# Performance work log

Hardware: AMD Instinct MI355X
Metric: run time of the kernel (lower is better)

## Reference

```python
import jax, jax.numpy as jnp
import numpy as np

DROP_PERCENT = 30  # a_percent passed in forward_construct_dynamic_ftr_map


def setup_inputs() -> dict:
    key = jax.random.key(0)
    # x: (b, w, n, h) = (batch, windows, nodes, feature/time)
    x = jax.random.normal(key, (8, 16, 400, 512), dtype=jnp.float32)
    return {"x": x}


def _dropedge(adj, percent):
    # adj: (B, n, n). Zero the `percent`% smallest-|value| entries per sample.
    # Matches torch's per-sample stable sort + scatter-zero, but batched.
    B, n, _ = adj.shape
    num_to_zero = int(n * n * percent / 100)
    if num_to_zero == 0:
        return adj
    flat = adj.reshape(B, n * n)
    # rank of each element in ascending |value| order (stable, like torch.sort)
    order = jnp.argsort(jnp.abs(flat), axis=-1)          # stable by default
    ranks = jnp.argsort(order, axis=-1)
    flat = jnp.where(ranks >= num_to_zero, flat, jnp.zeros((), flat.dtype))
    return flat.reshape(B, n, n)


def reference(x):
    b, w, n, h = x.shape
    xf = x.reshape(b * w, n, h)                 # rearrange 'b w n h -> (b w) n h'
    x_glb = xf.mean(axis=-1)                    # AdaptiveAvgPool1d(1)  -> (bw, n)
    x_max = xf.max(axis=-1)                     # AdaptiveMaxPool1d(1)  -> (bw, n)
    # bmm of (bw,n,1) @ (bw,1,n) == outer product per sample
    adj = jax.nn.sigmoid(x_glb[:, :, None] * x_max[:, None, :])  # (bw, n, n)
    dynamic_ftr_map = _dropedge(adj, DROP_PERCENT)
    return (xf, dynamic_ftr_map)
```

## Files before the change

### kernel.cpp

```cpp
#include <hip/hip_runtime.h>
#include <math.h>

#define HDIM  512
#define NSAMP 128
#define NN    400
#define NN2   160000
#define KZERO 48000
#define NROWS 51200
#define BPS   10
#define QPS   40000
#define QPB   4000
#define NBINS 12288
#define NWORDS 6144
#define BINBASE 0x3E000000u
#define BINSH 11
#define CANDCAP 1024

__device__ __forceinline__ float xla_expf(float x) {
  x = fminf(88.3762626647950f, fmaxf(-88.3762626647949f, x));
  float fx = floorf(fmaf(x, 1.44269504088896341f, 0.5f));
  x = fmaf(fx, -0.693359375f, x);
  x = fmaf(fx, 2.12194440e-4f, x);
  float z2 = __fmul_rn(x, x);
  float y = 1.9875691500e-4f;
  y = fmaf(y, x, 1.3981999507e-3f);
  y = fmaf(y, x, 8.3334519073e-3f);
  y = fmaf(y, x, 4.1665795894e-2f);
  y = fmaf(y, x, 1.6666665459e-1f);
  y = fmaf(y, x, 5.0000001201e-1f);
  y = fmaf(y, z2, x);
  y = __fadd_rn(y, 1.0f);
  int n = (int)fx;
  float p2n = __int_as_float((n + 127) << 23);
  return __fmul_rn(y, p2n);
}

__device__ __forceinline__ float sigf(float g, float m) {
  float z = __fmul_rn(g, m);
  float e = xla_expf(-z);
  float den = __fadd_rn(1.0f, e);
  return __fdiv_rn(1.0f, den);
}

__device__ __forceinline__ int binOf(unsigned int u) {
  if (u < BINBASE) return 0;
  unsigned int d = (u - BINBASE) >> BINSH;
  return d > (NBINS - 1) ? (NBINS - 1) : (int)d;
}

__global__ __launch_bounds__(256) void k_pool(const float* __restrict__ x,
                                              float* __restrict__ out0,
                                              float* __restrict__ glb,
                                              float* __restrict__ mx,
                                              unsigned int* __restrict__ zbase,
                                              int zwords) {
  int gid = blockIdx.x * 256 + threadIdx.x;
  if (gid < zwords) zbase[gid] = 0u;
  __shared__ float buf[4][512];
  const int wave = threadIdx.x >> 6;
  const int lane = threadIdx.x & 63;
  const int row  = blockIdx.x * 4 + wave;
  const float4* xr = reinterpret_cast<const float4*>(x) + (size_t)row * 128;
  float4* o = reinterpret_cast<float4*>(out0) + (size_t)row * 128;
  float4 a = xr[lane];
  float4 b = xr[lane + 64];
  o[lane]      = a;
  o[lane + 64] = b;
  reinterpret_cast<float4*>(buf[wave])[lane]      = a;
  reinterpret_cast<float4*>(buf[wave])[lane + 64] = b;
  float m = fmaxf(fmaxf(fmaxf(a.x, a.y), fmaxf(a.z, a.w)),
                  fmaxf(fmaxf(b.x, b.y), fmaxf(b.z, b.w)));
#pragma unroll
  for (int off = 32; off > 0; off >>= 1) m = fmaxf(m, __shfl_xor(m, off));
  __syncthreads();
  float r = 0.0f;
  if (lane < 8) {
    const float* p = buf[wave] + lane;
    r = p[0];
    for (int t = 1; t < 64; ++t) r = __fadd_rn(r, p[8 * t]);
    r = __fadd_rn(r, __shfl_xor(r, 4));
    r = __fadd_rn(r, __shfl_xor(r, 2));
    r = __fadd_rn(r, __shfl_xor(r, 1));
  }
  if (lane == 0) {
    glb[row] = __fmul_rn(r, 0.001953125f);
    mx[row]  = m;
  }
}

__global__ __launch_bounds__(256) void k_sig(const float* __restrict__ glb,
                                             const float* __restrict__ mx,
                                             unsigned int* __restrict__ adju,
                                             unsigned int* __restrict__ hist) {
  const int blk = blockIdx.x, b = blk / BPS, part = blk % BPS, t = threadIdx.x;
  __shared__ unsigned int lh[NWORDS];
  for (int k = t; k < NWORDS; k += 256) lh[k] = 0u;
  __syncthreads();
  const float* gb = glb + b * NN;
  const float4* mb = (const float4*)(mx + b * NN);
  uint4* base = (uint4*)adju + (size_t)b * QPS;
  const int qend = (part + 1) * QPB;
  for (int q = part * QPB + t; q < qend; q += 256) {
    int i  = q / 100;
    int jq = q - i * 100;
    float g = gb[i];
    float4 m4 = mb[jq];
    uint4 u;
    u.x = __float_as_uint(sigf(g, m4.x));
    u.y = __float_as_uint(sigf(g, m4.y));
    u.z = __float_as_uint(sigf(g, m4.z));
    u.w = __float_as_uint(sigf(g, m4.w));
    base[q] = u;
    int b0 = binOf(u.x), b1 = binOf(u.y), b2 = binOf(u.z), b3 = binOf(u.w);
    atomicAdd(&lh[b0 >> 1], 1u << ((b0 & 1) << 4));
    atomicAdd(&lh[b1 >> 1], 1u << ((b1 & 1) << 4));
    atomicAdd(&lh[b2 >> 1], 1u << ((b2 & 1) << 4));
    atomicAdd(&lh[b3 >> 1], 1u << ((b3 & 1) << 4));
  }
  __syncthreads();
  unsigned int* gh = hist + (size_t)b * NWORDS;
  for (int k = t; k < NWORDS; k += 256)
    if (lh[k]) atomicAdd(&gh[k], lh[k]);
}

__global__ __launch_bounds__(256) void k_scanBin(const unsigned int* __restrict__ hist,
                                                 unsigned int* __restrict__ stB,
                                                 unsigned int* __restrict__ stR) {
  const int b = blockIdx.x, t = threadIdx.x;
  const unsigned int* h = hist + (size_t)b * NWORDS;
  unsigned int w[24];
  unsigned int part = 0;
  for (int k = 0; k < 24; ++k) {
    w[k] = h[t * 24 + k];
    part += (w[k] & 0xffffu) + (w[k] >> 16);
  }
  const int lane = t & 63, wid = t >> 6;
  unsigned int inc = part;
  for (int off = 1; off < 64; off <<= 1) {
    unsigned int v = __shfl_up(inc, off);
    if (lane >= off) inc += v;
  }
  __shared__ unsigned int wsum[4], wbase[4];
  __shared__ int sB;
  __shared__ unsigned int sR;
  if (lane == 63) wsum[wid] = inc;
  __syncthreads();
  if (t == 0) {
    unsigned int c = 0;
    for (int i = 0; i < 4; ++i) { wbase[i] = c; c += wsum[i]; }
  }
  __syncthreads();
  unsigned int excl = wbase[wid] + inc - part;
  if (part > 0 && KZERO >= excl && KZERO < excl + part) {
    unsigned int c = excl;
    for (int k = 0; k < 24; ++k) {
      unsigned int lo = w[k] & 0xffffu, hi = w[k] >> 16;
      if ((unsigned)KZERO < c + lo) { sB = (t * 24 + k) * 2;     sR = KZERO - c; break; }
      c += lo;
      if ((unsigned)KZERO < c + hi) { sB = (t * 24 + k) * 2 + 1; sR = KZERO - c; break; }
      c += hi;
    }
  }
  __syncthreads();
  if (t == 0) { stB[b] = (unsigned int)sB; stR[b] = sR; }
}

__global__ __launch_bounds__(256) void k_cand(const unsigned int* __restrict__ adju,
                                              const unsigned int* __restrict__ stB,
                                              unsigned int* __restrict__ stNC,
                                              unsigned int* __restrict__ candI,
                                              unsigned int* __restrict__ candU) {
  const int blk = blockIdx.x, b = blk / BPS, part = blk % BPS, t = threadIdx.x;
  const int B = (int)stB[b];
  const uint4* base = (const uint4*)adju + (size_t)b * QPS;
  const int qend = (part + 1) * QPB;
  for (int q = part * QPB + t; q < qend; q += 256) {
    uint4 u = base[q];
    unsigned int uv[4] = {u.x, u.y, u.z, u.w};
#pragma unroll
    for (int k = 0; k < 4; ++k) {
      if (binOf(uv[k]) == B) {
        unsigned int pos = atomicAdd(&stNC[b], 1u);
        if (pos < CANDCAP) {
          candI[b * CANDCAP + pos] = (unsigned int)(q * 4 + k);
          candU[b * CANDCAP + pos] = uv[k];
        }
      }
    }
  }
}

__global__ __launch_bounds__(256) void k_final(unsigned int* __restrict__ adju,
                                               const unsigned int* __restrict__ stR,
                                               const unsigned int* __restrict__ stNC,
                                               const unsigned int* __restrict__ candI,
                                               const unsigned int* __restrict__ candU) {
  const int blk = blockIdx.x, b = blk / BPS, part = blk % BPS, t = threadIdx.x;
  __shared__ unsigned int cI[CANDCAP], cU[CANDCAP];
  __shared__ unsigned int sT, sIdx;
  int nc = (int)stNC[b];
  if (nc > CANDCAP) nc = CANDCAP;
  for (int i = t; i < nc; i += 256) {
    cI[i] = candI[b * CANDCAP + i];
    cU[i] = candU[b * CANDCAP + i];
  }
  if (t == 0) { sT = 0xFFFFFFFFu; sIdx = 0u; }
  __syncthreads();
  const unsigned int R = stR[b];
  for (int i = t; i < nc; i += 256) {
    unsigned int ui = cU[i], ii = cI[i];
    unsigned int rank = 0;
    for (int j = 0; j < nc; ++j)
      rank += (unsigned)((cU[j] < ui) || (cU[j] == ui && cI[j] < ii));
    if (rank == R) { sT = ui; sIdx = ii; }
  }
  __syncthreads();
  const unsigned int T = sT;
  const int idxT = (int)sIdx;
  uint4* base = (uint4*)adju + (size_t)b * QPS;
  const int qend = (part + 1) * QPB;
  for (int q = part * QPB + t; q < qend; q += 256) {
    uint4 u = base[q];
    int e0 = q * 4;
    uint4 v;
    v.x = (u.x < T || (u.x == T && (e0 + 0) < idxT)) ? 0u : u.x;
    v.y = (u.y < T || (u.y == T && (e0 + 1) < idxT)) ? 0u : u.y;
    v.z = (u.z < T || (u.z == T && (e0 + 2) < idxT)) ? 0u : u.z;
    v.w = (u.w < T || (u.w == T && (e0 + 3) < idxT)) ? 0u : u.w;
    if (v.x != u.x || v.y != u.y || v.z != u.z || v.w != u.w) base[q] = v;
  }
}

extern "C" void kernel_launch(void* const* d_in, const int* in_sizes, int n_in,
                              void* d_out, int out_size, void* d_ws, size_t ws_size,
                              hipStream_t stream) {
  const float* x = (const float*)d_in[0];
  float* out0 = (float*)d_out;
  unsigned int* adju = (unsigned int*)((float*)d_out + (size_t)26214400);

  char* ws = (char*)d_ws;
  float* glb = (float*)(ws + 0);
  float* mx  = (float*)(ws + 204800);
  unsigned int* hist = (unsigned int*)(ws + 409600);
  unsigned int* stNC = (unsigned int*)(ws + 3555328);
  unsigned int* stB  = (unsigned int*)(ws + 3555840);
  unsigned int* stR  = (unsigned int*)(ws + 3556352);
  unsigned int* candI = (unsigned int*)(ws + 3556864);
  unsigned int* candU = (unsigned int*)(ws + 4081152);
  unsigned int* zbase = hist;
  const int zwords = (3555840 - 409600) / 4;

  k_pool<<<NROWS / 4, 256, 0, stream>>>(x, out0, glb, mx, zbase, zwords);
  k_sig<<<NSAMP * BPS, 256, 0, stream>>>(glb, mx, adju, hist);
  k_scanBin<<<NSAMP, 256, 0, stream>>>(hist, stB, stR);
  k_cand<<<NSAMP * BPS, 256, 0, stream>>>(adju, stB, stNC, candI, candU);
  k_final<<<NSAMP * BPS, 256, 0, stream>>>(adju, stR, stNC, candI, candU);
}
```

Baseline: 121.8 us.

## Fuse bin scan into candidate pass and zero below-bin entries in same sweep

Folds the per-sample histogram scan into the candidate-collection kernel and into a new per-sample fix kernel, so the scan runs redundantly in each block instead of as a separate launch. The candidate pass now also zeroes every element whose bin lies below the threshold bin. The final kernel no longer rescans the whole adjacency; it only zeroes the candidates ranked below R. This removes one full read/write sweep of the 82MB adjacency and one launch, at the cost of redundant histogram scans per block.

```diff
diff --git a/kernel.cpp b/kernel.cpp
--- a/kernel.cpp
+++ b/kernel.cpp
@@ -123,18 +123,17 @@
     if (lh[k]) atomicAdd(&gh[k], lh[k]);
 }
 
-__global__ __launch_bounds__(256) void k_scanBin(const unsigned int* __restrict__ hist,
-                                                 unsigned int* __restrict__ stB,
-                                                 unsigned int* __restrict__ stR) {
-  const int b = blockIdx.x, t = threadIdx.x;
-  const unsigned int* h = hist + (size_t)b * NWORDS;
+__device__ __forceinline__ void scan_bin(const unsigned int* __restrict__ h,
+                                         int* B_out, unsigned int* R_out) {
+  const int t = threadIdx.x;
+  const int lane = t & 63, wid = t >> 6;
   unsigned int w[24];
   unsigned int part = 0;
+#pragma unroll
   for (int k = 0; k < 24; ++k) {
     w[k] = h[t * 24 + k];
     part += (w[k] & 0xffffu) + (w[k] >> 16);
   }
-  const int lane = t & 63, wid = t >> 6;
   unsigned int inc = part;
   for (int off = 1; off < 64; off <<= 1) {
     unsigned int v = __shfl_up(inc, off);
@@ -143,6 +142,7 @@
   __shared__ unsigned int wsum[4], wbase[4];
   __shared__ int sB;
   __shared__ unsigned int sR;
+  __syncthreads();
   if (lane == 63) wsum[wid] = inc;
   __syncthreads();
   if (t == 0) {
@@ -162,72 +162,63 @@
     }
   }
   __syncthreads();
-  if (t == 0) { stB[b] = (unsigned int)sB; stR[b] = sR; }
-}
-
-__global__ __launch_bounds__(256) void k_cand(const unsigned int* __restrict__ adju,
-                                              const unsigned int* __restrict__ stB,
-                                              unsigned int* __restrict__ stNC,
-                                              unsigned int* __restrict__ candI,
-                                              unsigned int* __restrict__ candU) {
+  *B_out = sB;
+  *R_out = sR;
+}
+
+__global__ __launch_bounds__(256) void k_candzero(unsigned int* __restrict__ adju,
+                                                  const unsigned int* __restrict__ hist,
+                                                  unsigned int* __restrict__ stNC,
+                                                  unsigned int* __restrict__ candI,
+                                                  unsigned int* __restrict__ candU) {
   const int blk = blockIdx.x, b = blk / BPS, part = blk % BPS, t = threadIdx.x;
-  const int B = (int)stB[b];
-  const uint4* base = (const uint4*)adju + (size_t)b * QPS;
+  int B; unsigned int R;
+  scan_bin(hist + (size_t)b * NWORDS, &B, &R);
+  uint4* base = (uint4*)adju + (size_t)b * QPS;
   const int qend = (part + 1) * QPB;
   for (int q = part * QPB + t; q < qend; q += 256) {
     uint4 u = base[q];
-    unsigned int uv[4] = {u.x, u.y, u.z, u.w};
-#pragma unroll
-    for (int k = 0; k < 4; ++k) {
-      if (binOf(uv[k]) == B) {
-        unsigned int pos = atomicAdd(&stNC[b], 1u);
-        if (pos < CANDCAP) {
-          candI[b * CANDCAP + pos] = (unsigned int)(q * 4 + k);
-          candU[b * CANDCAP + pos] = uv[k];
-        }
-      }
-    }
-  }
-}
-
-__global__ __launch_bounds__(256) void k_final(unsigned int* __restrict__ adju,
-                                               const unsigned int* __restrict__ stR,
-                                               const unsigned int* __restrict__ stNC,
-                                               const unsigned int* __restrict__ candI,
-                                               const unsigned int* __restrict__ candU) {
-  const int blk = blockIdx.x, b = blk / BPS, part = blk % BPS, t = threadIdx.x;
+    int b0 = binOf(u.x), b1 = binOf(u.y), b2 = binOf(u.z), b3 = binOf(u.w);
+    uint4 v = u;
+    if (b0 < B) v.x = 0u;
+    if (b1 < B) v.y = 0u;
+    if (b2 < B) v.z = 0u;
+    if (b3 < B) v.w = 0u;
+    if (b0 == B) { unsigned int p = atomicAdd(&stNC[b], 1u);
+      if (p < CANDCAP) { candI[b * CANDCAP + p] = (unsigned)(q * 4 + 0); candU[b * CANDCAP + p] = u.x; } }
+    if (b1 == B) { unsigned int p = atomicAdd(&stNC[b], 1u);
+      if (p < CANDCAP) { candI[b * CANDCAP + p] = (unsigned)(q * 4 + 1); candU[b * CANDCAP + p] = u.y; } }
+    if (b2 == B) { unsigned int p = atomicAdd(&stNC[b], 1u);
+      if (p < CANDCAP) { candI[b * CANDCAP + p] = (unsigned)(q * 4 + 2); candU[b * CANDCAP + p] = u.z; } }
+    if (b3 == B) { unsigned int p = atomicAdd(&stNC[b], 1u);
+      if (p < CANDCAP) { candI[b * CANDCAP + p] = (unsigned)(q * 4 + 3); candU[b * CANDCAP + p] = u.w; } }
+    if (v.x != u.x || v.y != u.y || v.z != u.z || v.w != u.w) base[q] = v;
+  }
+}
+
+__global__ __launch_bounds__(256) void k_fix(unsigned int* __restrict__ adju,
+                                             const unsigned int* __restrict__ hist,
+                                             const unsigned int* __restrict__ stNC,
+                                             const unsigned int* __restrict__ candI,
+                                             const unsigned int* __restrict__ candU) {
+  const int b = blockIdx.x, t = threadIdx.x;
+  int B; unsigned int R;
+  scan_bin(hist + (size_t)b * NWORDS, &B, &R);
   __shared__ unsigned int cI[CANDCAP], cU[CANDCAP];
-  __shared__ unsigned int sT, sIdx;
   int nc = (int)stNC[b];
   if (nc > CANDCAP) nc = CANDCAP;
   for (int i = t; i < nc; i += 256) {
     cI[i] = candI[b * CANDCAP + i];
     cU[i] = candU[b * CANDCAP + i];
   }
-  if (t == 0) { sT = 0xFFFFFFFFu; sIdx = 0u; }
-  __syncthreads();
-  const unsigned int R = stR[b];
+  __syncthreads();
+  unsigned int* a = adju + (size_t)b * NN2;
   for (int i = t; i < nc; i += 256) {
     unsigned int ui = cU[i], ii = cI[i];
     unsigned int rank = 0;
     for (int j = 0; j < nc; ++j)
       rank += (unsigned)((cU[j] < ui) || (cU[j] == ui && cI[j] < ii));
-    if (rank == R) { sT = ui; sIdx = ii; }
-  }
-  __syncthreads();
-  const unsigned int T = sT;
-  const int idxT = (int)sIdx;
-  uint4* base = (uint4*)adju + (size_t)b * QPS;
-  const int qend = (part + 1) * QPB;
-  for (int q = part * QPB + t; q < qend; q += 256) {
-    uint4 u = base[q];
-    int e0 = q * 4;
-    uint4 v;
-    v.x = (u.x < T || (u.x == T && (e0 + 0) < idxT)) ? 0u : u.x;
-    v.y = (u.y < T || (u.y == T && (e0 + 1) < idxT)) ? 0u : u.y;
-    v.z = (u.z < T || (u.z == T && (e0 + 2) < idxT)) ? 0u : u.z;
-    v.w = (u.w < T || (u.w == T && (e0 + 3) < idxT)) ? 0u : u.w;
-    if (v.x != u.x || v.y != u.y || v.z != u.z || v.w != u.w) base[q] = v;
+    if (rank < R) a[ii] = 0u;
   }
 }
 
@@ -243,16 +234,13 @@
   float* mx  = (float*)(ws + 204800);
   unsigned int* hist = (unsigned int*)(ws + 409600);
   unsigned int* stNC = (unsigned int*)(ws + 3555328);
-  unsigned int* stB  = (unsigned int*)(ws + 3555840);
-  unsigned int* stR  = (unsigned int*)(ws + 3556352);
-  unsigned int* candI = (unsigned int*)(ws + 3556864);
-  unsigned int* candU = (unsigned int*)(ws + 4081152);
+  unsigned int* candI = (unsigned int*)(ws + 3555840);
+  unsigned int* candU = (unsigned int*)(ws + 4080128);
   unsigned int* zbase = hist;
   const int zwords = (3555840 - 409600) / 4;
 
   k_pool<<<NROWS / 4, 256, 0, stream>>>(x, out0, glb, mx, zbase, zwords);
   k_sig<<<NSAMP * BPS, 256, 0, stream>>>(glb, mx, adju, hist);
-  k_scanBin<<<NSAMP, 256, 0, stream>>>(hist, stB, stR);
-  k_cand<<<NSAMP * BPS, 256, 0, stream>>>(adju, stB, stNC, candI, candU);
-  k_final<<<NSAMP * BPS, 256, 0, stream>>>(adju, stR, stNC, candI, candU);
-}
+  k_candzero<<<NSAMP * BPS, 256, 0, stream>>>(adju, hist, stNC, candI, candU);
+  k_fix<<<NSAMP, 256, 0, stream>>>(adju, hist, stNC, candI, candU);
+}
```

Result: faster. 110.8 us (-9.0%).
